# Optimization experiments

Hardware: AMD Instinct MI355X
Metric: run time of the kernel (lower is better)

Reference implementation:

```python
import jax, jax.numpy as jnp
import numpy as np

B, S, D = 4, 256, 2048
E, F, K = 32, 768, 8


def setup_inputs() -> dict:
    key = jax.random.key(0)
    k1, k2, k3, k4, k5 = jax.random.split(key, 5)
    sc_in = 1.0 / np.sqrt(D)
    sc_f = 1.0 / np.sqrt(F)
    return {
        "hidden_states": jax.random.normal(k1, (B, S, D), jnp.float32),
        "gate_w": jax.random.normal(k2, (E, D), jnp.float32) * sc_in,   # nn.Linear(D, E).weight
        "wg": jax.random.normal(k3, (E, F, D), jnp.float32) * sc_in,    # gate_proj weights [E, F, D]
        "wu": jax.random.normal(k4, (E, F, D), jnp.float32) * sc_in,    # up_proj weights   [E, F, D]
        "wd": jax.random.normal(k5, (E, D, F), jnp.float32) * sc_f,     # down_proj weights [E, D, F]
    }


def reference(hidden_states, gate_w, wg, wu, wd):
    b, s, d = hidden_states.shape
    x = hidden_states.reshape(-1, d)                        # [T, D]
    T = x.shape[0]

    # Router: linear -> softmax over experts -> top-k -> renormalize
    router_logits = jnp.einsum("td,ed->te", x, gate_w)      # [T, E]
    routing_probs = jax.nn.softmax(router_logits, axis=-1)
    topk_w, topk_idx = jax.lax.top_k(routing_probs, K)      # [T, K]
    topk_w = topk_w / jnp.sum(topk_w, axis=-1, keepdims=True)  # norm_topk_prob=True

    # Scatter top-k weights to dense [T, E] combine weights (zeros for unselected experts)
    combine = jnp.zeros((T, wg.shape[0]), x.dtype).at[
        jnp.arange(T)[:, None], topk_idx
    ].set(topk_w)                                           # [T, E]

    # Expert gated MLPs (computed for all experts, combined with sparse weights)
    g = jnp.einsum("td,efd->etf", x, wg)                    # [E, T, F]
    u = jnp.einsum("td,efd->etf", x, wu)                    # [E, T, F]
    h = jax.nn.silu(g) * u                                  # [E, T, F]
    y = jnp.einsum("etf,edf->etd", h, wd)                   # [E, T, D]

    out = jnp.einsum("te,etd->td", combine, y)              # [T, D]
    return out.reshape(b, s, d)
```

## Files before the change

### kernel.cpp

```cpp
#include <hip/hip_runtime.h>

#define T_TOK 1024
#define D_DIM 2048
#define E_NUM 32
#define F_DIM 768
#define K_TOP 8

typedef __bf16 v8bf __attribute__((ext_vector_type(8)));
typedef float v4f __attribute__((ext_vector_type(4)));
typedef unsigned short v8us __attribute__((ext_vector_type(8)));

__device__ __forceinline__ unsigned short f2b(float f) {
  unsigned int u = __builtin_bit_cast(unsigned int, f);
  u += 0x7fffu + ((u >> 16) & 1u);
  return (unsigned short)(u >> 16);
}
__device__ __forceinline__ float b2f(unsigned short s) {
  return __builtin_bit_cast(float, (unsigned int)s << 16);
}
__device__ __forceinline__ v8us cvt8u(v4f a, v4f b) {
  v8bf r;
  r[0] = (__bf16)a[0]; r[1] = (__bf16)a[1]; r[2] = (__bf16)a[2]; r[3] = (__bf16)a[3];
  r[4] = (__bf16)b[0]; r[5] = (__bf16)b[1]; r[6] = (__bf16)b[2]; r[7] = (__bf16)b[3];
  return __builtin_bit_cast(v8us, r);
}
__device__ __forceinline__ void gload16(const void* g, void* l) {
  __builtin_amdgcn_global_load_lds(
      (const __attribute__((address_space(1))) void*)g,
      (__attribute__((address_space(3))) void*)l, 16, 0, 0);
}
__device__ __forceinline__ v4f gload4f(const char* p) {
  v4f r;
  asm volatile("global_load_dwordx4 %0, %1, off" : "=v"(r) : "v"(p));
  return r;
}

#define VMWAIT(N) asm volatile("s_waitcnt vmcnt(" #N ")" ::: "memory")
#define LGKM0() asm volatile("s_waitcnt lgkmcnt(0)" ::: "memory")
#define SBAR() __builtin_amdgcn_s_barrier()
#define SCHEDB() __builtin_amdgcn_sched_barrier(0)

__global__ __launch_bounds__(256) void router_kernel(
    const float* __restrict__ x, const float* __restrict__ gw,
    unsigned short* __restrict__ xb, int* __restrict__ counts,
    int* __restrict__ tlist, int* __restrict__ topk_e, int* __restrict__ topk_p,
    float* __restrict__ topk_w, float* __restrict__ wlist)
{
  const int t = blockIdx.x, tid = threadIdx.x;
  const float* xr = x + (size_t)t * D_DIM;

  {
    v4f f0 = *reinterpret_cast<const v4f*>(xr + tid * 8);
    v4f f1 = *reinterpret_cast<const v4f*>(xr + tid * 8 + 4);
    *reinterpret_cast<v8us*>(xb + (size_t)t * D_DIM + tid * 8) = cvt8u(f0, f1);
  }

  __shared__ float logits[E_NUM];
  const int lane = tid & 63, wave = tid >> 6;
  const v4f* xr4 = reinterpret_cast<const v4f*>(xr);
  for (int j = 0; j < 8; ++j) {
    int e = wave * 8 + j;
    const v4f* wr4 = reinterpret_cast<const v4f*>(gw + (size_t)e * D_DIM);
    float s = 0.f;
#pragma unroll
    for (int i = 0; i < D_DIM / 256; ++i) {
      v4f a = xr4[lane + i * 64];
      v4f b = wr4[lane + i * 64];
      s = fmaf(a[0], b[0], s);
      s = fmaf(a[1], b[1], s);
      s = fmaf(a[2], b[2], s);
      s = fmaf(a[3], b[3], s);
    }
#pragma unroll
    for (int off = 32; off > 0; off >>= 1) s += __shfl_xor(s, off);
    if (lane == 0) logits[e] = s;
  }
  __syncthreads();

  if (tid == 0) {
    float lg[E_NUM];
#pragma unroll
    for (int e2 = 0; e2 < E_NUM; ++e2) lg[e2] = logits[e2];
    int sel[K_TOP]; float sv[K_TOP];
    for (int k = 0; k < K_TOP; ++k) {
      int best = 0; float bv = -3.4e38f;
      for (int e2 = 0; e2 < E_NUM; ++e2)
        if (lg[e2] > bv) { bv = lg[e2]; best = e2; }
      sel[k] = best; sv[k] = bv; lg[best] = -3.4e38f;
    }
    float mx = sv[0], s8 = 0.f, ww[K_TOP];
    for (int k = 0; k < K_TOP; ++k) { ww[k] = __expf(sv[k] - mx); s8 += ww[k]; }
    float inv = 1.f / s8;
    for (int k = 0; k < K_TOP; ++k) {
      float w = ww[k] * inv;
      int e2 = sel[k];
      int pos = atomicAdd(&counts[e2], 1);
      tlist[e2 * T_TOK + pos] = t;
      wlist[e2 * T_TOK + pos] = w;
      topk_e[t * K_TOP + k] = e2;
      topk_p[t * K_TOP + k] = pos;
      topk_w[t * K_TOP + k] = w;
    }
  }
}

__global__ void scan_kernel(const int* __restrict__ counts, int* __restrict__ offsets)
{
  if (threadIdx.x == 0) {
    int run = 0;
    for (int e = 0; e < E_NUM; ++e) { offsets[e] = run; run += counts[e]; }
  }
}

__global__ __launch_bounds__(512, 4) void gateup_kernel(
    const unsigned short* __restrict__ xb, const float* __restrict__ wg,
    const float* __restrict__ wu, const int* __restrict__ counts,
    const int* __restrict__ offsets, const int* __restrict__ tlist,
    unsigned short* __restrict__ hbuf)
{
  const int bid = blockIdx.x;
  const int xcd = bid & 7;
  const int j = bid >> 3;
  const int e = xcd + 8 * (j / 24);
  const int r = j % 24;
  const int tf = r >> 1;
  const int tm = r & 1;
  const int cnt = counts[e];
  if (tm * 192 >= cnt) return;

  __shared__ __align__(16) unsigned char lds[81920];

  const int tid = threadIdx.x;
  const int lane = tid & 63;
  const int wave = tid >> 6;
  const int wm = wave >> 1;
  const int wn = wave & 1;
  const int l15 = lane & 15;
  const int l4 = lane >> 4;

  const char* xbB = (const char*)xb;
  unsigned asrc[3], adst[3];
#pragma unroll
  for (int c = 0; c < 3; ++c) {
    int idx = tid + c * 512;
    int rr = idx >> 3, gl = idx & 7;
    int rg = tm * 192 + rr;
    if (rg > cnt - 1) rg = cnt - 1;
    int tok = tlist[e * T_TOK + rg];
    int gg = gl ^ (rr & 7);
    asrc[c] = (unsigned)tok * 4096u + (unsigned)(gg * 16);
    adst[c] = (unsigned)(idx * 16);
  }
  const int brow = tid >> 3, bg8 = tid & 7;
  const unsigned bsrc = (unsigned)((tf * 64 + brow) * 8192 + bg8 * 32);
  const unsigned bdst = (unsigned)(brow * 128 + ((bg8 ^ (brow & 7)) * 16));
  const char* gB = (const char*)wg + (size_t)e * F_DIM * D_DIM * 4;
  const char* uB = (const char*)wu + (size_t)e * F_DIM * D_DIM * 4;

  unsigned aRd[3];
#pragma unroll
  for (int fm = 0; fm < 3; ++fm) {
    int row = wm * 48 + fm * 16 + l15;
    aRd[fm] = (unsigned)(row * 128 + ((l4 ^ (row & 7)) * 16));
  }
  unsigned bRd[2];
#pragma unroll
  for (int fn = 0; fn < 2; ++fn) {
    int row = wn * 32 + fn * 16 + l15;
    bRd[fn] = (unsigned)(row * 128 + ((l4 ^ (row & 7)) * 16));
  }

  v4f zero = {0.f, 0.f, 0.f, 0.f};
  v4f accg[3][2], accu[3][2];
#pragma unroll
  for (int fm = 0; fm < 3; ++fm)
#pragma unroll
    for (int fn = 0; fn < 2; ++fn) { accg[fm][fn] = zero; accu[fm][fn] = zero; }

  auto COMPUTE = [&](unsigned ab, unsigned bb, unsigned sx) {
    v8bf af[3], bg[2], bu[2];
#pragma unroll
    for (int fm = 0; fm < 3; ++fm)
      af[fm] = __builtin_bit_cast(v8bf,
          *reinterpret_cast<const v8us*>(&lds[ab + (aRd[fm] ^ sx)]));
#pragma unroll
    for (int fn = 0; fn < 2; ++fn) {
      bg[fn] = __builtin_bit_cast(v8bf,
          *reinterpret_cast<const v8us*>(&lds[bb + (bRd[fn] ^ sx)]));
      bu[fn] = __builtin_bit_cast(v8bf,
          *reinterpret_cast<const v8us*>(&lds[bb + 8192u + (bRd[fn] ^ sx)]));
    }
#pragma unroll
    for (int fm = 0; fm < 3; ++fm)
#pragma unroll
      for (int fn = 0; fn < 2; ++fn) {
        accg[fm][fn] = __builtin_amdgcn_mfma_f32_16x16x32_bf16(af[fm], bg[fn], accg[fm][fn], 0, 0, 0);
        accu[fm][fn] = __builtin_amdgcn_mfma_f32_16x16x32_bf16(af[fm], bu[fn], accu[fm][fn], 0, 0, 0);
      }
  };

  const int NG = D_DIM / 64;

  v4f g0 = gload4f(gB + bsrc);
  v4f g1 = gload4f(gB + bsrc + 16);
  v4f u0 = gload4f(uB + bsrc);
  v4f u1 = gload4f(uB + bsrc + 16);
  SCHEDB();
#pragma unroll
  for (int c = 0; c < 3; ++c) gload16(xbB + asrc[c], &lds[adst[c]]);
  SCHEDB();

#pragma unroll 2
  for (int i = 0; i < NG; ++i) {
    const unsigned ab = (unsigned)(i & 1) * 24576u;
    const unsigned bb = 49152u + (unsigned)(i & 1) * 16384u;
    VMWAIT(3); SCHEDB();
    *reinterpret_cast<v8us*>(&lds[bb + bdst]) = cvt8u(g0, g1);
    *reinterpret_cast<v8us*>(&lds[bb + 8192u + bdst]) = cvt8u(u0, u1);
    if (i + 1 < NG) {
      const unsigned an = (unsigned)((i + 1) & 1) * 24576u;
      unsigned bo = bsrc + (unsigned)(i + 1) * 256u;
      g0 = gload4f(gB + bo);
      g1 = gload4f(gB + bo + 16);
      u0 = gload4f(uB + bo);
      u1 = gload4f(uB + bo + 16);
      SCHEDB();
      unsigned ao = (unsigned)(i + 1) * 128u;
#pragma unroll
      for (int c = 0; c < 3; ++c) gload16(xbB + asrc[c] + ao, &lds[an + adst[c]]);
      SCHEDB();
      VMWAIT(7);
    } else {
      VMWAIT(0);
    }
    SCHEDB(); LGKM0(); SBAR(); SCHEDB();
    COMPUTE(ab, bb, 0u);
    COMPUTE(ab, bb, 64u);
    SCHEDB(); SBAR();
  }

  const int off_e = offsets[e];
#pragma unroll
  for (int fm = 0; fm < 3; ++fm)
#pragma unroll
    for (int fn = 0; fn < 2; ++fn)
#pragma unroll
      for (int i = 0; i < 4; ++i) {
        int rloc = wm * 48 + fm * 16 + l4 * 4 + i;
        int rg = tm * 192 + rloc;
        if (rg < cnt) {
          int col = tf * 64 + wn * 32 + fn * 16 + l15;
          float g = accg[fm][fn][i];
          float uu = accu[fm][fn][i];
          float h = g * (1.f / (1.f + __expf(-g))) * uu;
          hbuf[(size_t)(off_e + rg) * F_DIM + col] = f2b(h);
        }
      }
}

template <int STAGEOUT>
__global__ __launch_bounds__(512, 4) void down_kernel(
    const unsigned short* __restrict__ hbuf, const float* __restrict__ wd,
    const int* __restrict__ counts, const int* __restrict__ offsets,
    const int* __restrict__ tlist, const float* __restrict__ wlist,
    unsigned short* __restrict__ ybuf, float* __restrict__ out)
{
  const int bid = blockIdx.x;
  const int xcd = bid & 7;
  const int j = bid >> 3;
  const int e = xcd + 8 * (j / 64);
  const int r = j % 64;
  const int td = r >> 1;
  const int tm = r & 1;
  const int cnt = counts[e];
  if (tm * 192 >= cnt) return;
  const int off_e = offsets[e];

  __shared__ __align__(16) unsigned char lds[65536];

  const int tid = threadIdx.x;
  const int lane = tid & 63;
  const int wave = tid >> 6;
  const int wm = wave >> 1;
  const int wn = wave & 1;
  const int l15 = lane & 15;
  const int l4 = lane >> 4;

  const char* hB = (const char*)hbuf;
  unsigned asrc[3], adst[3];
#pragma unroll
  for (int c = 0; c < 3; ++c) {
    int idx = tid + c * 512;
    int rr = idx >> 3, gl = idx & 7;
    int rg = tm * 192 + rr;
    if (rg > cnt - 1) rg = cnt - 1;
    int gg = gl ^ (rr & 7);
    asrc[c] = (unsigned)(off_e + rg) * 1536u + (unsigned)(gg * 16);
    adst[c] = (unsigned)(idx * 16);
  }
  const int brow = tid >> 3, bg8 = tid & 7;
  const unsigned bsrc = (unsigned)((td * 64 + brow) * 3072 + bg8 * 32);
  const unsigned bdst = (unsigned)(brow * 128 + ((bg8 ^ (brow & 7)) * 16));
  const char* bB = (const char*)wd + (size_t)e * D_DIM * F_DIM * 4;

  unsigned aRd[3];
#pragma unroll
  for (int fm = 0; fm < 3; ++fm) {
    int row = wm * 48 + fm * 16 + l15;
    aRd[fm] = (unsigned)(row * 128 + ((l4 ^ (row & 7)) * 16));
  }
  unsigned bRd[2];
#pragma unroll
  for (int fn = 0; fn < 2; ++fn) {
    int row = wn * 32 + fn * 16 + l15;
    bRd[fn] = (unsigned)(row * 128 + ((l4 ^ (row & 7)) * 16));
  }

  v4f zero = {0.f, 0.f, 0.f, 0.f};
  v4f acc[3][2];
#pragma unroll
  for (int fm = 0; fm < 3; ++fm)
#pragma unroll
    for (int fn = 0; fn < 2; ++fn) acc[fm][fn] = zero;

  auto COMPUTE = [&](unsigned ab, unsigned bb, unsigned sx) {
    v8bf af[3], bf_[2];
#pragma unroll
    for (int fm = 0; fm < 3; ++fm)
      af[fm] = __builtin_bit_cast(v8bf,
          *reinterpret_cast<const v8us*>(&lds[ab + (aRd[fm] ^ sx)]));
#pragma unroll
    for (int fn = 0; fn < 2; ++fn)
      bf_[fn] = __builtin_bit_cast(v8bf,
          *reinterpret_cast<const v8us*>(&lds[bb + (bRd[fn] ^ sx)]));
#pragma unroll
    for (int fm = 0; fm < 3; ++fm)
#pragma unroll
      for (int fn = 0; fn < 2; ++fn)
        acc[fm][fn] = __builtin_amdgcn_mfma_f32_16x16x32_bf16(af[fm], bf_[fn], acc[fm][fn], 0, 0, 0);
  };

  const int NG = F_DIM / 64;

  v4f b0 = gload4f(bB + bsrc);
  v4f b1 = gload4f(bB + bsrc + 16);
  SCHEDB();
#pragma unroll
  for (int c = 0; c < 3; ++c) gload16(hB + asrc[c], &lds[adst[c]]);
  SCHEDB();

#pragma unroll 2
  for (int i = 0; i < NG; ++i) {
    const unsigned ab = (unsigned)(i & 1) * 24576u;
    const unsigned bb = 49152u + (unsigned)(i & 1) * 8192u;
    VMWAIT(3); SCHEDB();
    *reinterpret_cast<v8us*>(&lds[bb + bdst]) = cvt8u(b0, b1);
    if (i + 1 < NG) {
      const unsigned an = (unsigned)((i + 1) & 1) * 24576u;
      unsigned bo = bsrc + (unsigned)(i + 1) * 256u;
      b0 = gload4f(bB + bo);
      b1 = gload4f(bB + bo + 16);
      SCHEDB();
      unsigned ao = (unsigned)(i + 1) * 128u;
#pragma unroll
      for (int c = 0; c < 3; ++c) gload16(hB + asrc[c] + ao, &lds[an + adst[c]]);
      SCHEDB();
      VMWAIT(5);
    } else {
      VMWAIT(0);
    }
    SCHEDB(); LGKM0(); SBAR(); SCHEDB();
    COMPUTE(ab, bb, 0u);
    COMPUTE(ab, bb, 64u);
    SCHEDB(); SBAR();
  }

#pragma unroll
  for (int fm = 0; fm < 3; ++fm)
#pragma unroll
    for (int fn = 0; fn < 2; ++fn)
#pragma unroll
      for (int i = 0; i < 4; ++i) {
        int rloc = wm * 48 + fm * 16 + l4 * 4 + i;
        int rg = tm * 192 + rloc;
        if (rg < cnt) {
          int col = td * 64 + wn * 32 + fn * 16 + l15;
          float y = acc[fm][fn][i];
          if (STAGEOUT) {
            ybuf[(size_t)(off_e + rg) * D_DIM + col] = f2b(y);
          } else {
            int tok = tlist[e * T_TOK + rg];
            float w = wlist[e * T_TOK + rg];
            atomicAdd(out + (size_t)tok * D_DIM + col, w * y);
          }
        }
      }
}

__global__ __launch_bounds__(256) void combine_kernel(
    const unsigned short* __restrict__ ybuf, const int* __restrict__ topk_e,
    const int* __restrict__ topk_p, const float* __restrict__ topk_w,
    const int* __restrict__ offsets, float* __restrict__ out)
{
  const int t = blockIdx.x, tid = threadIdx.x;
  const int d0 = tid * 8;
  float acc[8] = {0.f, 0.f, 0.f, 0.f, 0.f, 0.f, 0.f, 0.f};
#pragma unroll
  for (int k = 0; k < K_TOP; ++k) {
    int e = topk_e[t * K_TOP + k];
    int slot = offsets[e] + topk_p[t * K_TOP + k];
    float w = topk_w[t * K_TOP + k];
    v8us v = *reinterpret_cast<const v8us*>(ybuf + (size_t)slot * D_DIM + d0);
#pragma unroll
    for (int j = 0; j < 8; ++j) acc[j] += w * b2f(v[j]);
  }
  v4f o0 = {acc[0], acc[1], acc[2], acc[3]};
  v4f o1 = {acc[4], acc[5], acc[6], acc[7]};
  *reinterpret_cast<v4f*>(out + (size_t)t * D_DIM + d0) = o0;
  *reinterpret_cast<v4f*>(out + (size_t)t * D_DIM + d0 + 4) = o1;
}

extern "C" void kernel_launch(void* const* d_in, const int* in_sizes, int n_in,
                              void* d_out, int out_size, void* d_ws, size_t ws_size,
                              hipStream_t stream)
{
  const float* x  = (const float*)d_in[0];
  const float* gw = (const float*)d_in[1];
  const float* wg = (const float*)d_in[2];
  const float* wu = (const float*)d_in[3];
  const float* wd = (const float*)d_in[4];
  float* out = (float*)d_out;

  char* p = (char*)d_ws;
  auto alloc = [&](size_t bytes) {
    char* r = p;
    p += (bytes + 255) & ~(size_t)255;
    return r;
  };
  int* counts   = (int*)alloc(E_NUM * 4);
  int* offsets  = (int*)alloc(E_NUM * 4);
  int* tlist    = (int*)alloc((size_t)E_NUM * T_TOK * 4);
  float* wlist  = (float*)alloc((size_t)E_NUM * T_TOK * 4);
  int* topk_e   = (int*)alloc((size_t)T_TOK * K_TOP * 4);
  int* topk_p   = (int*)alloc((size_t)T_TOK * K_TOP * 4);
  float* topk_w = (float*)alloc((size_t)T_TOK * K_TOP * 4);
  unsigned short* xb   = (unsigned short*)alloc((size_t)T_TOK * D_DIM * 2);
  unsigned short* hbuf = (unsigned short*)alloc((size_t)T_TOK * K_TOP * F_DIM * 2);
  size_t need_atomic = (size_t)(p - (char*)d_ws);
  unsigned short* ybuf = (unsigned short*)alloc((size_t)T_TOK * K_TOP * D_DIM * 2);
  size_t need_stage = (size_t)(p - (char*)d_ws);

  if (ws_size < need_atomic) return;
  const bool stage = (ws_size >= need_stage);

  hipMemsetAsync(counts, 0, E_NUM * 4, stream);
  router_kernel<<<T_TOK, 256, 0, stream>>>(x, gw, xb, counts, tlist, topk_e, topk_p, topk_w, wlist);
  scan_kernel<<<1, 64, 0, stream>>>(counts, offsets);
  gateup_kernel<<<dim3(24 * E_NUM), 512, 0, stream>>>(
      xb, wg, wu, counts, offsets, tlist, hbuf);
  if (stage) {
    down_kernel<1><<<dim3(64 * E_NUM), 512, 0, stream>>>(
        hbuf, wd, counts, offsets, tlist, wlist, ybuf, out);
    combine_kernel<<<T_TOK, 256, 0, stream>>>(ybuf, topk_e, topk_p, topk_w, offsets, out);
  } else {
    hipMemsetAsync(out, 0, (size_t)out_size * 4, stream);
    down_kernel<0><<<dim3(64 * E_NUM), 512, 0, stream>>>(
        hbuf, wd, counts, offsets, tlist, wlist, ybuf, out);
  }
}
```

Measured before the change: 273.2 us.

## Halve gate/up block to 256 threads with doubled per-wave M tile

The gate/up GEMM kernel now runs with 256 threads (4 waves) instead of 512, and each wave covers 96 token rows (6 MFMA row tiles) instead of 48. The global loads and LDS staging of the weight tiles are redistributed so each thread handles 4 weight chunks and 6 activation chunks, with the vmcnt waits adjusted. The aim is more reuse of B fragments per wave and fewer waves competing for the same block, at the cost of doubled accumulator registers and lower occupancy, which may leave less latency hiding for the weight streaming.

```diff
diff --git a/kernel.cpp b/kernel.cpp
--- a/kernel.cpp
+++ b/kernel.cpp
@@ -112,7 +112,7 @@
   }
 }
 
-__global__ __launch_bounds__(512, 4) void gateup_kernel(
+__global__ __launch_bounds__(256, 2) void gateup_kernel(
     const unsigned short* __restrict__ xb, const float* __restrict__ wg,
     const float* __restrict__ wu, const int* __restrict__ counts,
     const int* __restrict__ offsets, const int* __restrict__ tlist,
@@ -139,10 +139,10 @@
   const int l4 = lane >> 4;
 
   const char* xbB = (const char*)xb;
-  unsigned asrc[3], adst[3];
-#pragma unroll
-  for (int c = 0; c < 3; ++c) {
-    int idx = tid + c * 512;
+  unsigned asrc[6], adst[6];
+#pragma unroll
+  for (int c = 0; c < 6; ++c) {
+    int idx = tid + c * 256;
     int rr = idx >> 3, gl = idx & 7;
     int rg = tm * 192 + rr;
     if (rg > cnt - 1) rg = cnt - 1;
@@ -151,16 +151,24 @@
     asrc[c] = (unsigned)tok * 4096u + (unsigned)(gg * 16);
     adst[c] = (unsigned)(idx * 16);
   }
-  const int brow = tid >> 3, bg8 = tid & 7;
-  const unsigned bsrc = (unsigned)((tf * 64 + brow) * 8192 + bg8 * 32);
-  const unsigned bdst = (unsigned)(brow * 128 + ((bg8 ^ (brow & 7)) * 16));
   const char* gB = (const char*)wg + (size_t)e * F_DIM * D_DIM * 4;
   const char* uB = (const char*)wu + (size_t)e * F_DIM * D_DIM * 4;
-
-  unsigned aRd[3];
-#pragma unroll
-  for (int fm = 0; fm < 3; ++fm) {
-    int row = wm * 48 + fm * 16 + l15;
+  const char* bp[4];
+  unsigned bdst[4];
+#pragma unroll
+  for (int c = 0; c < 4; ++c) {
+    int pidx = tid + c * 256;
+    int mat = pidx >= 512;
+    int mi = pidx & 511;
+    int row = mi >> 3, pr = mi & 7;
+    bp[c] = (mat ? uB : gB) + (size_t)(tf * 64 + row) * 8192 + pr * 32;
+    bdst[c] = (unsigned)(mat * 8192 + row * 128 + ((pr ^ (row & 7)) * 16));
+  }
+
+  unsigned aRd[6];
+#pragma unroll
+  for (int fm = 0; fm < 6; ++fm) {
+    int row = wm * 96 + fm * 16 + l15;
     aRd[fm] = (unsigned)(row * 128 + ((l4 ^ (row & 7)) * 16));
   }
   unsigned bRd[2];
@@ -171,16 +179,16 @@
   }
 
   v4f zero = {0.f, 0.f, 0.f, 0.f};
-  v4f accg[3][2], accu[3][2];
-#pragma unroll
-  for (int fm = 0; fm < 3; ++fm)
+  v4f accg[6][2], accu[6][2];
+#pragma unroll
+  for (int fm = 0; fm < 6; ++fm)
 #pragma unroll
     for (int fn = 0; fn < 2; ++fn) { accg[fm][fn] = zero; accu[fm][fn] = zero; }
 
   auto COMPUTE = [&](unsigned ab, unsigned bb, unsigned sx) {
-    v8bf af[3], bg[2], bu[2];
-#pragma unroll
-    for (int fm = 0; fm < 3; ++fm)
+    v8bf af[6], bg[2], bu[2];
+#pragma unroll
+    for (int fm = 0; fm < 6; ++fm)
       af[fm] = __builtin_bit_cast(v8bf,
           *reinterpret_cast<const v8us*>(&lds[ab + (aRd[fm] ^ sx)]));
 #pragma unroll
@@ -191,7 +199,7 @@
           *reinterpret_cast<const v8us*>(&lds[bb + 8192u + (bRd[fn] ^ sx)]));
     }
 #pragma unroll
-    for (int fm = 0; fm < 3; ++fm)
+    for (int fm = 0; fm < 6; ++fm)
 #pragma unroll
       for (int fn = 0; fn < 2; ++fn) {
         accg[fm][fn] = __builtin_amdgcn_mfma_f32_16x16x32_bf16(af[fm], bg[fn], accg[fm][fn], 0, 0, 0);
@@ -201,35 +209,33 @@
 
   const int NG = D_DIM / 64;
 
-  v4f g0 = gload4f(gB + bsrc);
-  v4f g1 = gload4f(gB + bsrc + 16);
-  v4f u0 = gload4f(uB + bsrc);
-  v4f u1 = gload4f(uB + bsrc + 16);
+  v4f b0[4], b1[4];
+#pragma unroll
+  for (int c = 0; c < 4; ++c) { b0[c] = gload4f(bp[c]); b1[c] = gload4f(bp[c] + 16); }
   SCHEDB();
 #pragma unroll
-  for (int c = 0; c < 3; ++c) gload16(xbB + asrc[c], &lds[adst[c]]);
+  for (int c = 0; c < 6; ++c) gload16(xbB + asrc[c], &lds[adst[c]]);
   SCHEDB();
 
 #pragma unroll 2
   for (int i = 0; i < NG; ++i) {
     const unsigned ab = (unsigned)(i & 1) * 24576u;
     const unsigned bb = 49152u + (unsigned)(i & 1) * 16384u;
-    VMWAIT(3); SCHEDB();
-    *reinterpret_cast<v8us*>(&lds[bb + bdst]) = cvt8u(g0, g1);
-    *reinterpret_cast<v8us*>(&lds[bb + 8192u + bdst]) = cvt8u(u0, u1);
+    VMWAIT(6); SCHEDB();
+#pragma unroll
+    for (int c = 0; c < 4; ++c)
+      *reinterpret_cast<v8us*>(&lds[bb + bdst[c]]) = cvt8u(b0[c], b1[c]);
     if (i + 1 < NG) {
       const unsigned an = (unsigned)((i + 1) & 1) * 24576u;
-      unsigned bo = bsrc + (unsigned)(i + 1) * 256u;
-      g0 = gload4f(gB + bo);
-      g1 = gload4f(gB + bo + 16);
-      u0 = gload4f(uB + bo);
-      u1 = gload4f(uB + bo + 16);
+      const unsigned ko = (unsigned)(i + 1) * 256u;
+#pragma unroll
+      for (int c = 0; c < 4; ++c) { b0[c] = gload4f(bp[c] + ko); b1[c] = gload4f(bp[c] + ko + 16); }
       SCHEDB();
-      unsigned ao = (unsigned)(i + 1) * 128u;
-#pragma unroll
-      for (int c = 0; c < 3; ++c) gload16(xbB + asrc[c] + ao, &lds[an + adst[c]]);
+      const unsigned ao = (unsigned)(i + 1) * 128u;
+#pragma unroll
+      for (int c = 0; c < 6; ++c) gload16(xbB + asrc[c] + ao, &lds[an + adst[c]]);
       SCHEDB();
-      VMWAIT(7);
+      VMWAIT(14);
     } else {
       VMWAIT(0);
     }
@@ -241,12 +247,12 @@
 
   const int off_e = offsets[e];
 #pragma unroll
-  for (int fm = 0; fm < 3; ++fm)
+  for (int fm = 0; fm < 6; ++fm)
 #pragma unroll
     for (int fn = 0; fn < 2; ++fn)
 #pragma unroll
       for (int i = 0; i < 4; ++i) {
-        int rloc = wm * 48 + fm * 16 + l4 * 4 + i;
+        int rloc = wm * 96 + fm * 16 + l4 * 4 + i;
         int rg = tm * 192 + rloc;
         if (rg < cnt) {
           int col = tf * 64 + wn * 32 + fn * 16 + l15;
@@ -456,7 +462,7 @@
   hipMemsetAsync(counts, 0, E_NUM * 4, stream);
   router_kernel<<<T_TOK, 256, 0, stream>>>(x, gw, xb, counts, tlist, topk_e, topk_p, topk_w, wlist);
   scan_kernel<<<1, 64, 0, stream>>>(counts, offsets);
-  gateup_kernel<<<dim3(24 * E_NUM), 512, 0, stream>>>(
+  gateup_kernel<<<dim3(24 * E_NUM), 256, 0, stream>>>(
       xb, wg, wu, counts, offsets, tlist, hbuf);
   if (stage) {
     down_kernel<1><<<dim3(64 * E_NUM), 512, 0, stream>>>(
```

Measured after the change: 348.4 us. 1.28x slower.
